# Performance work log

Hardware: AMD Instinct MI355X
Metric: run time of the kernel (lower is better)

## Reference

```python
import jax, jax.numpy as jnp
import numpy as np

N = 50000      # nodes
E = 800000     # edges (avg degree 16)
IN = 256       # in_feats
H = 128        # hidden_feats
C = 40         # out_feats == num classes (label dim)
LPA_ITERS = 10


def setup_inputs() -> dict:
    key = jax.random.key(0)
    ks = jax.random.split(key, 9)
    features = jax.random.normal(ks[0], (N, IN), dtype=jnp.float32)
    labels = jax.random.normal(ks[1], (N, C), dtype=jnp.float32)
    mask = jax.random.randint(ks[2], (N,), 0, 2) > 0          # bool [N]
    src = jax.random.randint(ks[3], (E,), 0, N, dtype=jnp.int32)
    dst = jax.random.randint(ks[4], (E,), 0, N, dtype=jnp.int32)
    W1 = jax.random.normal(ks[5], (IN, H), dtype=jnp.float32) * (1.0 / np.sqrt(IN))
    b1 = jnp.zeros((H,), dtype=jnp.float32)
    W2 = jax.random.normal(ks[6], (H, C), dtype=jnp.float32) * (1.0 / np.sqrt(H))
    b2 = jnp.zeros((C,), dtype=jnp.float32)
    return {"features": features, "labels": labels, "mask": mask,
            "src": src, "dst": dst, "W1": W1, "b1": b1, "W2": W2, "b2": b2}


def reference(features, labels, mask, src, dst, W1, b1, W2, b2):
    ones_e = jnp.ones((E,), dtype=jnp.float32)
    deg_out = jax.ops.segment_sum(ones_e, src, num_segments=N)  # out-degree
    deg_in = jax.ops.segment_sum(ones_e, dst, num_segments=N)   # in-degree
    norm_src = jnp.maximum(deg_out, 1.0) ** -0.5                 # DGL clamps deg>=1
    norm_dst = jnp.maximum(deg_in, 1.0) ** -0.5

    def gconv(x, W, b):
        # DGL GraphConv, norm='both': D_in^{-1/2} A^T D_out^{-1/2} (x W) + b
        h = (x @ W) * norm_src[:, None]                          # [N, d_out]
        agg = jax.ops.segment_sum(h[src], dst, num_segments=N)   # gather+scatter-add
        return agg * norm_dst[:, None] + b

    x = jax.nn.relu(gconv(features, W1, b1))
    # dropout identity in eval mode
    x = gconv(x, W2, b2)

    # Label propagation: adj[src,dst]=1 so (adj @ y)[i] = sum_{(i->j)} y[j]
    masked_labels = jnp.where(mask[:, None], labels, 0.0)

    def step(y, _):
        y = jax.ops.segment_sum(y[dst], src, num_segments=N)
        y = jnp.where(mask[:, None], labels, y)
        return y, None

    y, _ = jax.lax.scan(step, masked_labels, None, length=LPA_ITERS)
    return x, y
```

## Files before the change

### kernel.cpp

```cpp
#include <hip/hip_runtime.h>

#define Nn 50000
#define Ee 800000
#define INF_ 256
#define HID 128
#define NC 40
#define CAPD 48
#define CAPS 48
#define LPA_ITERS 10
#define NB 98
#define BSH 9
#define EPB 2048
#define NBLK ((Ee + EPB - 1) / EPB)
#define CAPB_D 10240
#define CAPB_S 6144

__device__ inline unsigned f2bf2(float a, float b) {
    unsigned ua = __float_as_uint(a); ua += 0x7FFFu + ((ua >> 16) & 1u);
    unsigned ub = __float_as_uint(b); ub += 0x7FFFu + ((ub >> 16) & 1u);
    return (ua >> 16) | (ub & 0xFFFF0000u);
}
__device__ inline float bf_lo(unsigned u) { return __uint_as_float(u << 16); }
__device__ inline float bf_hi(unsigned u) { return __uint_as_float(u & 0xFFFF0000u); }

__global__ void detect_fmt(const unsigned int* __restrict__ m, int* flag) {
    int i = blockIdx.x * blockDim.x + threadIdx.x;
    if (i < 12500) {
        if (m[i] > 1u) atomicOr(flag, 1);
    }
}

__device__ inline bool read_mask(const void* mask, int node, int fmt) {
    if (fmt) return ((const unsigned char*)mask)[node] != 0;
    return ((const int*)mask)[node] != 0;
}

__global__ __launch_bounds__(256) void bin_edges(
    const int* __restrict__ src, const int* __restrict__ dst,
    const void* __restrict__ mask, const int* __restrict__ flag,
    int* __restrict__ cnt_src,
    int* __restrict__ cur_d, int* __restrict__ cur_s,
    unsigned* __restrict__ bkt_d, unsigned* __restrict__ bkt_s) {
    __shared__ unsigned stage_d[EPB];
    __shared__ unsigned stage_s[EPB];
    __shared__ int hd[NB], od[NB + 1], cd[NB], gd_[NB];
    __shared__ int hs[NB], os_[NB + 1], cs_[NB], gs_[NB];
    int tid = threadIdx.x;
    int e0 = blockIdx.x * EPB;
    int fmt = *flag;
    if (tid < NB) { hd[tid] = 0; hs[tid] = 0; }
    __syncthreads();

    int rs[EPB / 256], rd[EPB / 256];
    unsigned um = 0;
#pragma unroll
    for (int k = 0; k < EPB / 256; k++) {
        int e = e0 + tid + k * 256;
        rs[k] = -1; rd[k] = -1;
        if (e < Ee) {
            int s = src[e], d = dst[e];
            rs[k] = s; rd[k] = d;
            atomicAdd(&cnt_src[s], 1);
            atomicAdd(&hd[d >> BSH], 1);
            if (!read_mask(mask, s, fmt)) {
                um |= (1u << k);
                atomicAdd(&hs[s >> BSH], 1);
            }
        }
    }
    __syncthreads();
    if (tid == 0) {
        int run = 0;
        for (int b = 0; b < NB; b++) { od[b] = run; run += hd[b]; }
        od[NB] = run;
        run = 0;
        for (int b = 0; b < NB; b++) { os_[b] = run; run += hs[b]; }
        os_[NB] = run;
    }
    __syncthreads();
    if (tid < NB) {
        gd_[tid] = hd[tid] ? atomicAdd(&cur_d[tid], hd[tid]) : 0;
        gs_[tid] = hs[tid] ? atomicAdd(&cur_s[tid], hs[tid]) : 0;
        cd[tid] = od[tid];
        cs_[tid] = os_[tid];
    }
    __syncthreads();
#pragma unroll
    for (int k = 0; k < EPB / 256; k++) {
        if (rd[k] >= 0) {
            int p = atomicAdd(&cd[rd[k] >> BSH], 1);
            stage_d[p] = ((unsigned)rd[k] << 16) | (unsigned)rs[k];
            if (um & (1u << k)) {
                int q = atomicAdd(&cs_[rs[k] >> BSH], 1);
                stage_s[q] = ((unsigned)rs[k] << 16) | (unsigned)rd[k];
            }
        }
    }
    __syncthreads();
    int totd = od[NB];
    for (int i = tid; i < totd; i += 256) {
        int lo = 0, hi = NB;
        while (hi - lo > 1) {
            int mid = (lo + hi) >> 1;
            if (od[mid] <= i) lo = mid; else hi = mid;
        }
        int pos = gd_[lo] + (i - od[lo]);
        if (pos < CAPB_D) bkt_d[(size_t)lo * CAPB_D + pos] = stage_d[i];
    }
    int tots = os_[NB];
    for (int i = tid; i < tots; i += 256) {
        int lo = 0, hi = NB;
        while (hi - lo > 1) {
            int mid = (lo + hi) >> 1;
            if (os_[mid] <= i) lo = mid; else hi = mid;
        }
        int pos = gs_[lo] + (i - os_[lo]);
        if (pos < CAPB_S) bkt_s[(size_t)lo * CAPB_S + pos] = stage_s[i];
    }
}

__global__ __launch_bounds__(256) void build_csr_dst(
    const unsigned* __restrict__ bkt, const int* __restrict__ cur,
    int* __restrict__ adj, int* __restrict__ cnt) {
    __shared__ int lc[512];
    int b = blockIdx.x, tid = threadIdx.x;
    lc[tid] = 0; lc[tid + 256] = 0;
    __syncthreads();
    int n = cur[b]; if (n > CAPB_D) n = CAPB_D;
    int n0 = b << BSH;
    const unsigned* base = bkt + (size_t)b * CAPB_D;
    for (int i = tid; i < n; i += 256) {
        unsigned r = base[i];
        int d = r >> 16, s = r & 0xffff;
        int sl = atomicAdd(&lc[d - n0], 1);
        if (sl < CAPD) adj[d * CAPD + sl] = s;
    }
    __syncthreads();
    int g0 = n0 + tid;
    if (g0 < Nn) cnt[g0] = lc[tid];
    g0 += 256;
    if (g0 < Nn) cnt[g0] = lc[tid + 256];
}

__global__ __launch_bounds__(256) void build_csr_src(
    const unsigned* __restrict__ bkt, const int* __restrict__ cur,
    const void* __restrict__ mask, const int* __restrict__ flag,
    int* __restrict__ adj, int* __restrict__ cnt_u, int* __restrict__ cnt_m) {
    __shared__ int lu[512], lm[512];
    int b = blockIdx.x, tid = threadIdx.x;
    lu[tid] = 0; lu[tid + 256] = 0; lm[tid] = 0; lm[tid + 256] = 0;
    __syncthreads();
    int fmt = *flag;
    int n = cur[b]; if (n > CAPB_S) n = CAPB_S;
    int n0 = b << BSH;
    const unsigned* base = bkt + (size_t)b * CAPB_S;
    for (int i = tid; i < n; i += 256) {
        unsigned r = base[i];
        int s = r >> 16, d = r & 0xffff;
        if (read_mask(mask, d, fmt)) {
            int sl = atomicAdd(&lm[s - n0], 1);
            if (sl < CAPS) adj[s * CAPS + (CAPS - 1 - sl)] = d;
        } else {
            int sl = atomicAdd(&lu[s - n0], 1);
            if (sl < CAPS) adj[s * CAPS + sl] = d;
        }
    }
    __syncthreads();
    int g0 = n0 + tid;
    if (g0 < Nn) { cnt_u[g0] = lu[tid]; cnt_m[g0] = lm[tid]; }
    g0 += 256;
    if (g0 < Nn) { cnt_u[g0] = lu[tid + 256]; cnt_m[g0] = lm[tid + 256]; }
}

__global__ void build_unmasked(const void* __restrict__ mask,
                               const int* __restrict__ flag,
                               int* n_un, int* __restrict__ ulist) {
    int i = blockIdx.x * blockDim.x + threadIdx.x;
    if (i < Nn) {
        if (!read_mask(mask, i, *flag)) {
            int p = atomicAdd(n_un, 1);
            ulist[p] = i;
        }
    }
}

#define G1_ROWS 64
#define G1_KT 32
__global__ __launch_bounds__(256) void gemm1(
    const float* __restrict__ feat, const float* __restrict__ W1,
    const int* __restrict__ cnt_src, unsigned* __restrict__ h1b) {
    __shared__ float4 lA4[G1_ROWS][8];
    __shared__ float lB[G1_KT][HID];
    const int tid = threadIdx.x;
    const int row0 = blockIdx.x * G1_ROWS;
    const int r0 = (tid >> 5) * 8;
    const int c0 = (tid & 31) * 4;

    float4 acc[8];
#pragma unroll
    for (int i = 0; i < 8; i++) acc[i] = make_float4(0.f, 0.f, 0.f, 0.f);

    for (int k0 = 0; k0 < INF_; k0 += G1_KT) {
#pragma unroll
        for (int p = 0; p < 2; p++) {
            int idx = tid + p * 256;
            int r = idx >> 3, c = idx & 7;
            int grow = row0 + r;
            float4 v = make_float4(0.f, 0.f, 0.f, 0.f);
            if (grow < Nn)
                v = *(const float4*)(feat + (size_t)grow * INF_ + k0 + c * 4);
            lA4[r][c] = v;
        }
#pragma unroll
        for (int p = 0; p < 4; p++) {
            int idx = tid + p * 256;
            int kb = idx >> 5, c4 = idx & 31;
            *(float4*)(&lB[kb][c4 * 4]) =
                *(const float4*)(W1 + (size_t)(k0 + kb) * HID + c4 * 4);
        }
        __syncthreads();
#pragma unroll
        for (int k4 = 0; k4 < 8; k4++) {
            float4 av[8];
#pragma unroll
            for (int i = 0; i < 8; i++) av[i] = lA4[r0 + i][k4];
#pragma unroll
            for (int kk = 0; kk < 4; kk++) {
                float4 bv = *(const float4*)(&lB[k4 * 4 + kk][c0]);
#pragma unroll
                for (int i = 0; i < 8; i++) {
                    float a = kk == 0 ? av[i].x
                            : kk == 1 ? av[i].y
                            : kk == 2 ? av[i].z : av[i].w;
                    acc[i].x += a * bv.x; acc[i].y += a * bv.y;
                    acc[i].z += a * bv.z; acc[i].w += a * bv.w;
                }
            }
        }
        __syncthreads();
    }
#pragma unroll
    for (int i = 0; i < 8; i++) {
        int grow = row0 + r0 + i;
        if (grow < Nn) {
            int dg = cnt_src[grow];
            float nrm = rsqrtf((float)(dg > 1 ? dg : 1));
            uint2 pk;
            pk.x = f2bf2(acc[i].x * nrm, acc[i].y * nrm);
            pk.y = f2bf2(acc[i].z * nrm, acc[i].w * nrm);
            *(uint2*)(h1b + (size_t)grow * 64 + (c0 >> 1)) = pk;
        }
    }
}

__global__ __launch_bounds__(256) void agg_relu1(
    const uint4* __restrict__ h1b, const int* __restrict__ adj_dst,
    const int* __restrict__ cnt_dst, const float4* __restrict__ b1,
    float4* __restrict__ x1) {
    int node = blockIdx.x * 16 + (threadIdx.x >> 4);
    int l = threadIdx.x & 15;
    int dg = cnt_dst[node];
    int cnt = dg < CAPD ? dg : CAPD;
    const int* lst = adj_dst + (size_t)node * CAPD;
    float s0 = 0.f, s1 = 0.f, s2 = 0.f, s3 = 0.f;
    float s4 = 0.f, s5 = 0.f, s6 = 0.f, s7 = 0.f;
    int e = 0;
    for (; e + 8 <= cnt; e += 8) {
        uint4 u[8];
#pragma unroll
        for (int q = 0; q < 8; q++) u[q] = h1b[(size_t)lst[e + q] * 16 + l];
#pragma unroll
        for (int q = 0; q < 8; q++) {
            s0 += bf_lo(u[q].x); s1 += bf_hi(u[q].x);
            s2 += bf_lo(u[q].y); s3 += bf_hi(u[q].y);
            s4 += bf_lo(u[q].z); s5 += bf_hi(u[q].z);
            s6 += bf_lo(u[q].w); s7 += bf_hi(u[q].w);
        }
    }
    for (; e < cnt; e++) {
        uint4 u = h1b[(size_t)lst[e] * 16 + l];
        s0 += bf_lo(u.x); s1 += bf_hi(u.x);
        s2 += bf_lo(u.y); s3 += bf_hi(u.y);
        s4 += bf_lo(u.z); s5 += bf_hi(u.z);
        s6 += bf_lo(u.w); s7 += bf_hi(u.w);
    }
    float nrm = rsqrtf((float)(dg > 1 ? dg : 1));
    float4 bb0 = b1[l * 2], bb1 = b1[l * 2 + 1];
    float4 v0, v1;
    v0.x = fmaxf(s0 * nrm + bb0.x, 0.f);
    v0.y = fmaxf(s1 * nrm + bb0.y, 0.f);
    v0.z = fmaxf(s2 * nrm + bb0.z, 0.f);
    v0.w = fmaxf(s3 * nrm + bb0.w, 0.f);
    v1.x = fmaxf(s4 * nrm + bb1.x, 0.f);
    v1.y = fmaxf(s5 * nrm + bb1.y, 0.f);
    v1.z = fmaxf(s6 * nrm + bb1.z, 0.f);
    v1.w = fmaxf(s7 * nrm + bb1.w, 0.f);
    x1[(size_t)node * 32 + l * 2] = v0;
    x1[(size_t)node * 32 + l * 2 + 1] = v1;
}

__global__ __launch_bounds__(256) void gemm2(
    const float4* __restrict__ x1, const float4* __restrict__ W2,
    const int* __restrict__ cnt_src, unsigned* __restrict__ h2b) {
    __shared__ float lw[HID * NC];
    int tid = threadIdx.x;
    for (int i = tid; i < HID * NC / 4; i += 256)
        ((float4*)lw)[i] = W2[i];
    __syncthreads();
    int r = blockIdx.x * 256 + tid;
    if (r >= Nn) return;
    const float4* xr = x1 + (size_t)r * 32;
    float4 acc[10];
#pragma unroll
    for (int j = 0; j < 10; j++) acc[j] = make_float4(0.f, 0.f, 0.f, 0.f);
    for (int k4 = 0; k4 < 32; k4++) {
        float4 xv = xr[k4];
#pragma unroll
        for (int s = 0; s < 4; s++) {
            float x = s == 0 ? xv.x : (s == 1 ? xv.y : (s == 2 ? xv.z : xv.w));
            const float4* wrow = (const float4*)(lw + (k4 * 4 + s) * NC);
#pragma unroll
            for (int j = 0; j < 10; j++) {
                float4 w = wrow[j];
                acc[j].x += x * w.x; acc[j].y += x * w.y;
                acc[j].z += x * w.z; acc[j].w += x * w.w;
            }
        }
    }
    int dg = cnt_src[r];
    float nrm = rsqrtf((float)(dg > 1 ? dg : 1));
    uint2* out = (uint2*)(h2b + (size_t)r * 20);
#pragma unroll
    for (int j = 0; j < 10; j++) {
        uint2 pk;
        pk.x = f2bf2(acc[j].x * nrm, acc[j].y * nrm);
        pk.y = f2bf2(acc[j].z * nrm, acc[j].w * nrm);
        out[j] = pk;
    }
}

__global__ __launch_bounds__(320) void agg2(
    const uint2* __restrict__ h2b, const int* __restrict__ adj_dst,
    const int* __restrict__ cnt_dst, const float4* __restrict__ b2,
    float4* __restrict__ out_x) {
    int node = blockIdx.x * 32 + threadIdx.x / 10;
    int l = threadIdx.x % 10;
    if (node >= Nn) return;
    int dg = cnt_dst[node];
    int cnt = dg < CAPD ? dg : CAPD;
    const int* lst = adj_dst + (size_t)node * CAPD;
    float s0 = 0.f, s1 = 0.f, s2 = 0.f, s3 = 0.f;
    int e = 0;
    for (; e + 8 <= cnt; e += 8) {
        uint2 u[8];
#pragma unroll
        for (int q = 0; q < 8; q++) u[q] = h2b[(size_t)lst[e + q] * 10 + l];
#pragma unroll
        for (int q = 0; q < 8; q++) {
            s0 += bf_lo(u[q].x); s1 += bf_hi(u[q].x);
            s2 += bf_lo(u[q].y); s3 += bf_hi(u[q].y);
        }
    }
    for (; e + 4 <= cnt; e += 4) {
        uint2 u[4];
#pragma unroll
        for (int q = 0; q < 4; q++) u[q] = h2b[(size_t)lst[e + q] * 10 + l];
#pragma unroll
        for (int q = 0; q < 4; q++) {
            s0 += bf_lo(u[q].x); s1 += bf_hi(u[q].x);
            s2 += bf_lo(u[q].y); s3 += bf_hi(u[q].y);
        }
    }
    for (; e < cnt; e++) {
        uint2 u = h2b[(size_t)lst[e] * 10 + l];
        s0 += bf_lo(u.x); s1 += bf_hi(u.x);
        s2 += bf_lo(u.y); s3 += bf_hi(u.y);
    }
    float nrm = rsqrtf((float)(dg > 1 ? dg : 1));
    float4 bb = b2[l];
    float4 v;
    v.x = s0 * nrm + bb.x;
    v.y = s1 * nrm + bb.y;
    v.z = s2 * nrm + bb.z;
    v.w = s3 * nrm + bb.w;
    out_x[(size_t)node * 10 + l] = v;
}

__global__ void lpa_init(const float* __restrict__ labels, const void* mask,
                         const int* __restrict__ flag, float* __restrict__ out_y) {
    int g = blockIdx.x * blockDim.x + threadIdx.x;
    if (g >= Nn * NC) return;
    int node = g / NC;
    if (read_mask(mask, node, *flag)) out_y[g] = labels[g];
}

__global__ __launch_bounds__(320) void lpa_const(
    const float4* __restrict__ labels, const int* __restrict__ n_un,
    const int* __restrict__ ulist, const int* __restrict__ adj_s,
    const int* __restrict__ cnt_m, float4* __restrict__ sconst,
    uint2* __restrict__ y1b) {
    int g = blockIdx.x * 32 + threadIdx.x / 10;
    int l = threadIdx.x % 10;
    if (g >= *n_un) return;
    int u = ulist[g];
    int cm = cnt_m[u];
    int cnt = cm < CAPS ? cm : CAPS;
    const int* lst = adj_s + (size_t)u * CAPS + (CAPS - cnt);
    float4 s = make_float4(0.f, 0.f, 0.f, 0.f);
    int e = 0;
    for (; e + 8 <= cnt; e += 8) {
        float4 v[8];
#pragma unroll
        for (int q = 0; q < 8; q++) v[q] = labels[(size_t)lst[e + q] * 10 + l];
#pragma unroll
        for (int q = 0; q < 8; q++) {
            s.x += v[q].x; s.y += v[q].y; s.z += v[q].z; s.w += v[q].w;
        }
    }
    for (; e + 4 <= cnt; e += 4) {
        float4 v[4];
#pragma unroll
        for (int q = 0; q < 4; q++) v[q] = labels[(size_t)lst[e + q] * 10 + l];
#pragma unroll
        for (int q = 0; q < 4; q++) {
            s.x += v[q].x; s.y += v[q].y; s.z += v[q].z; s.w += v[q].w;
        }
    }
    for (; e < cnt; e++) {
        float4 a = labels[(size_t)lst[e] * 10 + l];
        s.x += a.x; s.y += a.y; s.z += a.z; s.w += a.w;
    }
    sconst[(size_t)u * 10 + l] = s;
    uint2 pk; pk.x = f2bf2(s.x, s.y); pk.y = f2bf2(s.z, s.w);
    y1b[(size_t)u * 10 + l] = pk;
}

__global__ __launch_bounds__(320) void lpa_mid(
    const uint2* __restrict__ ycur, const int* __restrict__ n_un,
    const int* __restrict__ ulist, const int* __restrict__ adj_s,
    const int* __restrict__ cnt_u, const float4* __restrict__ sconst,
    uint2* __restrict__ ynext) {
    int g = blockIdx.x * 32 + threadIdx.x / 10;
    int l = threadIdx.x % 10;
    if (g >= *n_un) return;
    int u = ulist[g];
    int cu = cnt_u[u];
    int cnt = cu < CAPS ? cu : CAPS;
    const int* lst = adj_s + (size_t)u * CAPS;
    float4 s = sconst[(size_t)u * 10 + l];
    int e = 0;
    for (; e + 8 <= cnt; e += 8) {
        uint2 v[8];
#pragma unroll
        for (int q = 0; q < 8; q++) v[q] = ycur[(size_t)lst[e + q] * 10 + l];
#pragma unroll
        for (int q = 0; q < 8; q++) {
            s.x += bf_lo(v[q].x); s.y += bf_hi(v[q].x);
            s.z += bf_lo(v[q].y); s.w += bf_hi(v[q].y);
        }
    }
    for (; e + 4 <= cnt; e += 4) {
        uint2 v[4];
#pragma unroll
        for (int q = 0; q < 4; q++) v[q] = ycur[(size_t)lst[e + q] * 10 + l];
#pragma unroll
        for (int q = 0; q < 4; q++) {
            s.x += bf_lo(v[q].x); s.y += bf_hi(v[q].x);
            s.z += bf_lo(v[q].y); s.w += bf_hi(v[q].y);
        }
    }
    for (; e < cnt; e++) {
        uint2 v = ycur[(size_t)lst[e] * 10 + l];
        s.x += bf_lo(v.x); s.y += bf_hi(v.x);
        s.z += bf_lo(v.y); s.w += bf_hi(v.y);
    }
    uint2 pk; pk.x = f2bf2(s.x, s.y); pk.y = f2bf2(s.z, s.w);
    ynext[(size_t)u * 10 + l] = pk;
}

__global__ __launch_bounds__(320) void lpa_last(
    const uint2* __restrict__ ycur, const int* __restrict__ n_un,
    const int* __restrict__ ulist, const int* __restrict__ adj_s,
    const int* __restrict__ cnt_u, const float4* __restrict__ sconst,
    float4* __restrict__ out_y) {
    int g = blockIdx.x * 32 + threadIdx.x / 10;
    int l = threadIdx.x % 10;
    if (g >= *n_un) return;
    int u = ulist[g];
    int cu = cnt_u[u];
    int cnt = cu < CAPS ? cu : CAPS;
    const int* lst = adj_s + (size_t)u * CAPS;
    float4 s = sconst[(size_t)u * 10 + l];
    int e = 0;
    for (; e + 8 <= cnt; e += 8) {
        uint2 v[8];
#pragma unroll
        for (int q = 0; q < 8; q++) v[q] = ycur[(size_t)lst[e + q] * 10 + l];
#pragma unroll
        for (int q = 0; q < 8; q++) {
            s.x += bf_lo(v[q].x); s.y += bf_hi(v[q].x);
            s.z += bf_lo(v[q].y); s.w += bf_hi(v[q].y);
        }
    }
    for (; e + 4 <= cnt; e += 4) {
        uint2 v[4];
#pragma unroll
        for (int q = 0; q < 4; q++) v[q] = ycur[(size_t)lst[e + q] * 10 + l];
#pragma unroll
        for (int q = 0; q < 4; q++) {
            s.x += bf_lo(v[q].x); s.y += bf_hi(v[q].x);
            s.z += bf_lo(v[q].y); s.w += bf_hi(v[q].y);
        }
    }
    for (; e < cnt; e++) {
        uint2 v = ycur[(size_t)lst[e] * 10 + l];
        s.x += bf_lo(v.x); s.y += bf_hi(v.x);
        s.z += bf_lo(v.y); s.w += bf_hi(v.y);
    }
    out_y[(size_t)u * 10 + l] = s;
}

extern "C" void kernel_launch(void* const* d_in, const int* in_sizes, int n_in,
                              void* d_out, int out_size, void* d_ws, size_t ws_size,
                              hipStream_t stream) {
    const float* feat   = (const float*)d_in[0];
    const float* labels = (const float*)d_in[1];
    const void*  mask   = d_in[2];
    const int*   src    = (const int*)d_in[3];
    const int*   dst    = (const int*)d_in[4];
    const float* W1     = (const float*)d_in[5];
    const float* b1     = (const float*)d_in[6];
    const float* W2     = (const float*)d_in[7];
    const float* b2     = (const float*)d_in[8];

    float* out_x = (float*)d_out;
    float* out_y = out_x + (size_t)Nn * NC;

    char* ws = (char*)d_ws;
    size_t off = 0;
    auto alloc = [&](size_t bytes) -> void* {
        void* p = ws + off;
        off += (bytes + 255) & ~(size_t)255;
        return p;
    };
    int* flag    = (int*)alloc(256);
    int* n_un    = flag + 1;
    int* cnt_src = (int*)alloc((size_t)Nn * 4);
    int* cur_d   = (int*)alloc(512);
    int* cur_s   = (int*)alloc(512);
    size_t zero_bytes = off;
    int* cnt_dst = (int*)alloc((size_t)Nn * 4);
    int* cnt_u   = (int*)alloc((size_t)Nn * 4);
    int* cnt_m   = (int*)alloc((size_t)Nn * 4);
    int* ulist   = (int*)alloc((size_t)Nn * 4);
    char* uni = (char*)alloc((size_t)Nn * HID * 2);
    unsigned* bkt_d = (unsigned*)uni;
    unsigned* bkt_s = (unsigned*)(uni + (size_t)NB * CAPB_D * 4);
    unsigned* h1b = (unsigned*)uni;
    float* x1 = (float*)alloc((size_t)Nn * HID * 4);
    int* adj_s   = (int*)alloc((size_t)Nn * CAPS * 4);
    int* adj_dst = (int*)alloc((size_t)Nn * CAPD * 4);
    unsigned* h2b = (unsigned*)alloc((size_t)Nn * NC * 2);
    float* sconst = (float*)alloc((size_t)Nn * NC * 4);
    uint2* y1b = (uint2*)alloc((size_t)Nn * NC * 2);
    uint2* y2b = (uint2*)alloc((size_t)Nn * NC * 2);

    hipMemsetAsync(d_ws, 0, zero_bytes, stream);

    detect_fmt<<<49, 256, 0, stream>>>((const unsigned int*)mask, flag);
    bin_edges<<<NBLK, 256, 0, stream>>>(src, dst, mask, flag, cnt_src,
                                        cur_d, cur_s, bkt_d, bkt_s);
    build_csr_dst<<<NB, 256, 0, stream>>>(bkt_d, cur_d, adj_dst, cnt_dst);
    build_csr_src<<<NB, 256, 0, stream>>>(bkt_s, cur_s, mask, flag,
                                          adj_s, cnt_u, cnt_m);
    build_unmasked<<<196, 256, 0, stream>>>(mask, flag, n_un, ulist);

    gemm1<<<(Nn + G1_ROWS - 1) / G1_ROWS, 256, 0, stream>>>(feat, W1, cnt_src, h1b);
    agg_relu1<<<Nn / 16, 256, 0, stream>>>((const uint4*)h1b, adj_dst, cnt_dst,
                                           (const float4*)b1, (float4*)x1);
    gemm2<<<196, 256, 0, stream>>>((const float4*)x1, (const float4*)W2,
                                   cnt_src, h2b);
    agg2<<<(Nn + 31) / 32, 320, 0, stream>>>((const uint2*)h2b, adj_dst, cnt_dst,
                                             (const float4*)b2, (float4*)out_x);

    lpa_init<<<(Nn * NC + 255) / 256, 256, 0, stream>>>(labels, mask, flag, out_y);
    lpa_const<<<(Nn + 31) / 32, 320, 0, stream>>>(
        (const float4*)labels, n_un, ulist, adj_s, cnt_m, (float4*)sconst, y1b);
    const uint2* cur = y1b;
    for (int i = 0; i < 8; i++) {
        uint2* nxt = (i & 1) ? y1b : y2b;
        lpa_mid<<<(Nn + 31) / 32, 320, 0, stream>>>(
            cur, n_un, ulist, adj_s, cnt_u, (const float4*)sconst, nxt);
        cur = nxt;
    }
    lpa_last<<<(Nn + 31) / 32, 320, 0, stream>>>(
        cur, n_un, ulist, adj_s, cnt_u, (const float4*)sconst, (float4*)out_y);
}
```

Baseline: 430.9 us.

## Use bf16 MFMA for first-layer GEMM with pre-transposed bf16 weights

Rewrites gemm1 to convert feature tiles to bf16 in shared memory and compute with 16x16x32 bf16 MFMA instructions instead of scalar FP32 FMAs. A small prep kernel transposes W1 into bf16 column-major layout so B fragments load contiguously. This targets the FP32 ALU cost of the 50000x256x128 product but reduces input precision to bf16. The output stores are now scalar 16-bit writes, which are less coalesced than before.

```diff
diff --git a/kernel.cpp b/kernel.cpp
--- a/kernel.cpp
+++ b/kernel.cpp
@@ -15,10 +15,17 @@
 #define CAPB_D 10240
 #define CAPB_S 6144
 
+typedef __attribute__((ext_vector_type(8))) short bfrag;
+typedef __attribute__((ext_vector_type(4))) float ffrag;
+
 __device__ inline unsigned f2bf2(float a, float b) {
     unsigned ua = __float_as_uint(a); ua += 0x7FFFu + ((ua >> 16) & 1u);
     unsigned ub = __float_as_uint(b); ub += 0x7FFFu + ((ub >> 16) & 1u);
     return (ua >> 16) | (ub & 0xFFFF0000u);
+}
+__device__ inline unsigned short f2bf(float a) {
+    unsigned ua = __float_as_uint(a); ua += 0x7FFFu + ((ua >> 16) & 1u);
+    return (unsigned short)(ua >> 16);
 }
 __device__ inline float bf_lo(unsigned u) { return __uint_as_float(u << 16); }
 __device__ inline float bf_hi(unsigned u) { return __uint_as_float(u & 0xFFFF0000u); }
@@ -184,71 +191,77 @@
     }
 }
 
+__global__ void prep_w1t(const float* __restrict__ W1,
+                         unsigned short* __restrict__ W1t) {
+    int c = blockIdx.x;
+    int k = threadIdx.x;
+    W1t[c * INF_ + k] = f2bf(W1[(size_t)k * HID + c]);
+}
+
 #define G1_ROWS 64
-#define G1_KT 32
 __global__ __launch_bounds__(256) void gemm1(
-    const float* __restrict__ feat, const float* __restrict__ W1,
-    const int* __restrict__ cnt_src, unsigned* __restrict__ h1b) {
-    __shared__ float4 lA4[G1_ROWS][8];
-    __shared__ float lB[G1_KT][HID];
+    const float* __restrict__ feat, const unsigned short* __restrict__ W1t,
+    const int* __restrict__ cnt_src, unsigned short* __restrict__ h1b) {
+    __shared__ unsigned short lA[G1_ROWS * 32];
+    __shared__ unsigned short lB[HID * 32];
     const int tid = threadIdx.x;
     const int row0 = blockIdx.x * G1_ROWS;
-    const int r0 = (tid >> 5) * 8;
-    const int c0 = (tid & 31) * 4;
-
-    float4 acc[8];
-#pragma unroll
-    for (int i = 0; i < 8; i++) acc[i] = make_float4(0.f, 0.f, 0.f, 0.f);
-
-    for (int k0 = 0; k0 < INF_; k0 += G1_KT) {
+    const int w = tid >> 6;
+    const int l = tid & 63;
+    const int lane15 = l & 15;
+    const int quad = l >> 4;
+    const int rw0 = w * 16;
+
+    ffrag acc[8];
+#pragma unroll
+    for (int t = 0; t < 8; t++) acc[t] = (ffrag){0.f, 0.f, 0.f, 0.f};
+
+    for (int k0 = 0; k0 < INF_; k0 += 32) {
 #pragma unroll
         for (int p = 0; p < 2; p++) {
             int idx = tid + p * 256;
-            int r = idx >> 3, c = idx & 7;
+            int r = idx >> 3, c4 = idx & 7;
             int grow = row0 + r;
             float4 v = make_float4(0.f, 0.f, 0.f, 0.f);
             if (grow < Nn)
-                v = *(const float4*)(feat + (size_t)grow * INF_ + k0 + c * 4);
-            lA4[r][c] = v;
-        }
-#pragma unroll
-        for (int p = 0; p < 4; p++) {
+                v = *(const float4*)(feat + (size_t)grow * INF_ + k0 + c4 * 4);
+            uint2 pk;
+            pk.x = f2bf2(v.x, v.y);
+            pk.y = f2bf2(v.z, v.w);
+            *(uint2*)((char*)lA + r * 64 + c4 * 8) = pk;
+        }
+#pragma unroll
+        for (int p = 0; p < 2; p++) {
             int idx = tid + p * 256;
-            int kb = idx >> 5, c4 = idx & 31;
-            *(float4*)(&lB[kb][c4 * 4]) =
-                *(const float4*)(W1 + (size_t)(k0 + kb) * HID + c4 * 4);
+            int col = idx >> 2, q = idx & 3;
+            uint4 v = *(const uint4*)((const char*)W1t + col * 512 + k0 * 2 + q * 16);
+            *(uint4*)((char*)lB + col * 64 + q * 16) = v;
         }
         __syncthreads();
-#pragma unroll
-        for (int k4 = 0; k4 < 8; k4++) {
-            float4 av[8];
-#pragma unroll
-            for (int i = 0; i < 8; i++) av[i] = lA4[r0 + i][k4];
-#pragma unroll
-            for (int kk = 0; kk < 4; kk++) {
-                float4 bv = *(const float4*)(&lB[k4 * 4 + kk][c0]);
-#pragma unroll
-                for (int i = 0; i < 8; i++) {
-                    float a = kk == 0 ? av[i].x
-                            : kk == 1 ? av[i].y
-                            : kk == 2 ? av[i].z : av[i].w;
-                    acc[i].x += a * bv.x; acc[i].y += a * bv.y;
-                    acc[i].z += a * bv.z; acc[i].w += a * bv.w;
-                }
-            }
+        int arow = rw0 + lane15;
+        bfrag af = *(const bfrag*)((const char*)lA + arow * 64 + quad * 16);
+#pragma unroll
+        for (int t = 0; t < 8; t++) {
+            int col = t * 16 + lane15;
+            bfrag bf = *(const bfrag*)((const char*)lB + col * 64 + quad * 16);
+            acc[t] = __builtin_amdgcn_mfma_f32_16x16x32_bf16(af, bf, acc[t], 0, 0, 0);
         }
         __syncthreads();
     }
-#pragma unroll
-    for (int i = 0; i < 8; i++) {
-        int grow = row0 + r0 + i;
-        if (grow < Nn) {
-            int dg = cnt_src[grow];
-            float nrm = rsqrtf((float)(dg > 1 ? dg : 1));
-            uint2 pk;
-            pk.x = f2bf2(acc[i].x * nrm, acc[i].y * nrm);
-            pk.y = f2bf2(acc[i].z * nrm, acc[i].w * nrm);
-            *(uint2*)(h1b + (size_t)grow * 64 + (c0 >> 1)) = pk;
+    float nrm[4];
+#pragma unroll
+    for (int i = 0; i < 4; i++) {
+        int grow = row0 + rw0 + quad * 4 + i;
+        int dg = (grow < Nn) ? cnt_src[grow] : 1;
+        nrm[i] = rsqrtf((float)(dg > 1 ? dg : 1));
+    }
+#pragma unroll
+    for (int t = 0; t < 8; t++) {
+#pragma unroll
+        for (int i = 0; i < 4; i++) {
+            int grow = row0 + rw0 + quad * 4 + i;
+            if (grow < Nn)
+                h1b[(size_t)grow * HID + t * 16 + lane15] = f2bf(acc[t][i] * nrm[i]);
         }
     }
 }
@@ -553,10 +566,11 @@
     int* cnt_u   = (int*)alloc((size_t)Nn * 4);
     int* cnt_m   = (int*)alloc((size_t)Nn * 4);
     int* ulist   = (int*)alloc((size_t)Nn * 4);
+    unsigned short* W1t = (unsigned short*)alloc((size_t)HID * INF_ * 2);
     char* uni = (char*)alloc((size_t)Nn * HID * 2);
     unsigned* bkt_d = (unsigned*)uni;
     unsigned* bkt_s = (unsigned*)(uni + (size_t)NB * CAPB_D * 4);
-    unsigned* h1b = (unsigned*)uni;
+    unsigned short* h1b = (unsigned short*)uni;
     float* x1 = (float*)alloc((size_t)Nn * HID * 4);
     int* adj_s   = (int*)alloc((size_t)Nn * CAPS * 4);
     int* adj_dst = (int*)alloc((size_t)Nn * CAPD * 4);
@@ -568,6 +582,7 @@
     hipMemsetAsync(d_ws, 0, zero_bytes, stream);
 
     detect_fmt<<<49, 256, 0, stream>>>((const unsigned int*)mask, flag);
+    prep_w1t<<<HID, INF_, 0, stream>>>(W1, W1t);
     bin_edges<<<NBLK, 256, 0, stream>>>(src, dst, mask, flag, cnt_src,
                                         cur_d, cur_s, bkt_d, bkt_s);
     build_csr_dst<<<NB, 256, 0, stream>>>(bkt_d, cur_d, adj_dst, cnt_dst);
@@ -575,7 +590,7 @@
                                           adj_s, cnt_u, cnt_m);
     build_unmasked<<<196, 256, 0, stream>>>(mask, flag, n_un, ulist);
 
-    gemm1<<<(Nn + G1_ROWS - 1) / G1_ROWS, 256, 0, stream>>>(feat, W1, cnt_src, h1b);
+    gemm1<<<(Nn + G1_ROWS - 1) / G1_ROWS, 256, 0, stream>>>(feat, W1t, cnt_src, h1b);
     agg_relu1<<<Nn / 16, 256, 0, stream>>>((const uint4*)h1b, adj_dst, cnt_dst,
                                            (const float4*)b1, (float4*)x1);
     gemm2<<<196, 256, 0, stream>>>((const float4*)x1, (const float4*)W2,
```

After: 398.2 us. 1.08x faster.
